# Kernel tuning notes

Hardware: AMD Instinct MI355X
Metric: run time of the kernel (lower is better)

The kernel has to match this reference:

```python
import jax, jax.numpy as jnp
import numpy as np

EPS_D = 1e-05
EPS_LOG = 1e-05
H_BAND = 0.5


def setup_inputs() -> dict:
    key = jax.random.key(0)
    k1, k2 = jax.random.split(key)
    N, C, Hh, Ww = 4, 256, 64, 64
    y = jax.random.normal(k1, (N, C, Hh, Ww), dtype=jnp.float32)
    y_hat = jax.random.normal(k2, (N, C, Hh, Ww), dtype=jnp.float32)
    return {"y": y, "y_hat": y_hat}


def contextual_loss(x, y, h=H_BAND):
    # x, y: (N, C, H, W)
    N, C, Hh, Ww = x.shape
    # mean over W, H, N of y -> per-channel mu, broadcast as (1, C, 1, 1)
    y_mu = y.mean(axis=3).mean(axis=2).mean(axis=0).reshape(1, C, 1, 1)
    x_c = x - y_mu
    y_c = y - y_mu
    x_n = x_c / jnp.linalg.norm(x_c, ord=2, axis=1, keepdims=True)
    y_n = y_c / jnp.linalg.norm(y_c, ord=2, axis=1, keepdims=True)
    x_n = x_n.reshape(N, C, Hh * Ww)  # (N, C, P)
    y_n = y_n.reshape(N, C, Hh * Ww)
    # cosine similarity: (N, P, P)
    cosine_sim = jnp.einsum('ncp,ncq->npq', x_n, y_n)
    d = 1.0 - cosine_sim
    d_min = jnp.min(d, axis=2, keepdims=True)
    d_tilde = d / (d_min + EPS_D)
    w = jnp.exp((1.0 - d_tilde) / h)
    cx_ij = w / jnp.sum(w, axis=2, keepdims=True)
    cx = jnp.mean(jnp.max(cx_ij, axis=1), axis=1)  # (N,)
    return jnp.mean(-jnp.log(cx + EPS_LOG))


def reference(y, y_hat):
    return contextual_loss(y, y_hat)
```

## Files before the change

kernel.cpp:

```cpp
#include <hip/hip_runtime.h>
#include <hip/hip_bf16.h>
#include <math.h>


namespace {
constexpr int NB = 4;
constexpr int C  = 256;
constexpr int P  = 4096;
constexpr float EPSD = 1e-5f;
constexpr float EPSL = 1e-5f;
constexpr float HB   = 0.5f;

constexpr size_t OFF_MU    = 0;
constexpr size_t OFF_XNT   = 256;
constexpr size_t OFF_YNT   = OFF_XNT + (size_t)NB * P * C / 2;
constexpr size_t OFF_XS    = OFF_YNT + (size_t)NB * P * C / 2;
constexpr size_t OFF_RMAXH = OFF_XS + (size_t)NB * P * C / 2;
constexpr size_t OFF_SUMH  = OFF_RMAXH + (size_t)NB * 4 * P;
constexpr size_t OFF_CMAXH = OFF_SUMH + (size_t)NB * 4 * P;
constexpr size_t OFF_RMAX  = OFF_CMAXH + (size_t)NB * 4 * P;
constexpr size_t OFF_ALPHA = OFF_RMAX + (size_t)NB * P;
constexpr size_t OFF_LROW  = OFF_ALPHA + (size_t)NB * P;
}

typedef __attribute__((ext_vector_type(8))) __bf16 bf16x8;
typedef __attribute__((ext_vector_type(16))) float f32x16;
typedef unsigned short u16;

__device__ __forceinline__ bf16x8 ldfrag(const u16* p) {
  return *reinterpret_cast<const bf16x8*>(p);
}
__device__ __forceinline__ void gload_lds16(const u16* g, u16* l) {
  __builtin_amdgcn_global_load_lds(
      (const __attribute__((address_space(1))) void*)g,
      (__attribute__((address_space(3))) void*)l, 16, 0, 0);
}
__device__ __forceinline__ f32x16 zero16() {
  f32x16 z;
#pragma unroll
  for (int i = 0; i < 16; ++i) z[i] = 0.f;
  return z;
}

__device__ __forceinline__ void stage_tile64(const u16* __restrict__ src, int row0,
                                             u16* lds, int t) {
#pragma unroll
  for (int i = 0; i < 8; ++i) {
    const int g  = i * 256 + t;
    const int r  = g >> 5;
    const int gs = (g & 31) ^ (r & 15);
    gload_lds16(src + (size_t)(row0 + r) * 256 + gs * 8, lds + (size_t)g * 8);
  }
}

__global__ void k_mu(const float* __restrict__ yh, float* __restrict__ ws) {
  const int c = blockIdx.x;
  const int t = threadIdx.x;
  float s = 0.f;
  for (int n = 0; n < NB; ++n) {
    const float* base = yh + ((size_t)(n * C + c)) * P;
    for (int p = t; p < P; p += 256) s += base[p];
  }
  __shared__ float red[256];
  red[t] = s;
  __syncthreads();
  for (int w = 128; w > 0; w >>= 1) {
    if (t < w) red[t] += red[t + w];
    __syncthreads();
  }
  if (t == 0) ws[OFF_MU + c] = red[0] * (1.0f / (NB * P));
}

__global__ __launch_bounds__(256) void k_norm(const float* __restrict__ x,
                                              const float* __restrict__ yh,
                                              float* __restrict__ ws) {
  const int b     = blockIdx.x;
  const int arr   = b & 1;
  const int strip = (b >> 1) & 63;
  const int n     = b >> 7;
  const int t     = threadIdx.x;
  const int w     = t >> 6;
  const int l     = t & 63;

  __shared__ float mu_s[C];
  __shared__ float tile[64][257];
  __shared__ float red[4][64];
  __shared__ float invs[64];

  mu_s[t] = ws[OFF_MU + t];
  __syncthreads();

  const float* src = arr ? yh : x;
  const size_t base = ((size_t)n * C) * P + (size_t)strip * 64 + l;
  float ssq = 0.f;
  for (int cc = 0; cc < C; cc += 4) {
    const int c = cc + w;
    const float v = src[base + (size_t)c * P] - mu_s[c];
    tile[l][c] = v;
    ssq += v * v;
  }
  red[w][l] = ssq;
  __syncthreads();
  if (t < 64) invs[t] = 1.0f / sqrtf(red[0][t] + red[1][t] + red[2][t] + red[3][t]);
  __syncthreads();

  uint* dst = reinterpret_cast<uint*>(ws + (arr ? OFF_YNT : OFF_XNT));
  const int c2 = t & 127;
  const size_t drow = ((size_t)n * P + (size_t)strip * 64) * (C / 2);
  for (int it = 0; it < 32; ++it) {
    const int pl = it * 2 + (t >> 7);
    const float s  = invs[pl];
    const float v0 = tile[pl][2 * c2] * s;
    const float v1 = tile[pl][2 * c2 + 1] * s;
    const unsigned short u0 = __builtin_bit_cast(unsigned short, __float2bfloat16(v0));
    const unsigned short u1 = __builtin_bit_cast(unsigned short, __float2bfloat16(v1));
    dst[drow + (size_t)pl * (C / 2) + c2] = ((uint)u1 << 16) | u0;
  }
}

template <int PASS>
__global__ __launch_bounds__(256, 1) void k_rows(float* __restrict__ ws) {
  const int t = threadIdx.x;
  const int wave = t >> 6, l = t & 63, l31 = l & 31, lh = l >> 5, l15 = l31 & 15;
  const int rt = wave >> 1, ct = wave & 1;
  const int bid = blockIdx.x;
  const int qp = bid & 3, n = (bid >> 2) & 3, strip = bid >> 4;
  const int p0 = strip * 128;
  const int qbase = qp * 1024;

  const u16* A = reinterpret_cast<const u16*>(ws + (PASS == 0 ? OFF_XNT : OFF_XS)) +
                 (size_t)n * P * C;
  const u16* yn = reinterpret_cast<const u16*>(ws + OFF_YNT) + (size_t)n * P * C;

  __shared__ __align__(16) u16 Bl[2][64 * 256];

  const u16* Ap0 = A + (size_t)(p0 + rt * 64 + l31) * 256;
  bf16x8 af0[16], af1[16];
#pragma unroll
  for (int ks = 0; ks < 16; ++ks) {
    af0[ks] = ldfrag(Ap0 + (ks * 2 + lh) * 8);
    af1[ks] = ldfrag(Ap0 + 32 * 256 + (ks * 2 + lh) * 8);
  }
  asm volatile("s_waitcnt vmcnt(0)" ::: "memory");
  __builtin_amdgcn_sched_barrier(0);

  float run0[16], run1[16];
#pragma unroll
  for (int r = 0; r < 16; ++r) {
    run0[r] = (PASS == 0) ? -3.0e38f : 0.f;
    run1[r] = (PASS == 0) ? -3.0e38f : 0.f;
  }

  stage_tile64(yn, qbase, Bl[0], t);

  for (int step = 0; step < 16; ++step) {
    if (step + 1 < 16) {
      stage_tile64(yn, qbase + (step + 1) * 64, Bl[(step + 1) & 1], t);
      asm volatile("s_waitcnt vmcnt(8)" ::: "memory");
    } else {
      asm volatile("s_waitcnt vmcnt(0)" ::: "memory");
    }
    __builtin_amdgcn_sched_barrier(0);
    __builtin_amdgcn_s_barrier();
    __builtin_amdgcn_sched_barrier(0);

    const u16* Brow = &Bl[step & 1][(size_t)(ct * 32 + l31) * 256];
    f32x16 a0 = zero16(), a1 = zero16();
    __builtin_amdgcn_s_setprio(1);
#pragma unroll
    for (int ks = 0; ks < 16; ++ks) {
      const bf16x8 bq = ldfrag(Brow + ((ks * 2 + lh) ^ l15) * 8);
      a0 = __builtin_amdgcn_mfma_f32_32x32x16_bf16(af0[ks], bq, a0, 0, 0, 0);
      a1 = __builtin_amdgcn_mfma_f32_32x32x16_bf16(af1[ks], bq, a1, 0, 0, 0);
    }
    __builtin_amdgcn_s_setprio(0);

    if (PASS == 0) {
#pragma unroll
      for (int r = 0; r < 16; ++r) {
        run0[r] = fmaxf(run0[r], a0[r]);
        run1[r] = fmaxf(run1[r], a1[r]);
      }
    } else {
#pragma unroll
      for (int r = 0; r < 16; ++r) {
        run0[r] += __expf(a0[r]);
        run1[r] += __expf(a1[r]);
      }
    }
    __builtin_amdgcn_sched_barrier(0);
    __builtin_amdgcn_s_barrier();
  }

#pragma unroll
  for (int m = 1; m <= 16; m <<= 1) {
#pragma unroll
    for (int r = 0; r < 16; ++r) {
      const float o0 = __shfl_xor(run0[r], m, 64);
      const float o1 = __shfl_xor(run1[r], m, 64);
      run0[r] = (PASS == 0) ? fmaxf(run0[r], o0) : (run0[r] + o0);
      run1[r] = (PASS == 0) ? fmaxf(run1[r], o1) : (run1[r] + o1);
    }
  }
  float (*red)[64] = reinterpret_cast<float(*)[64]>(&Bl[0][0]);
  if (l31 == 0) {
#pragma unroll
    for (int r = 0; r < 16; ++r) {
      const int row = (r & 3) + 8 * (r >> 2) + 4 * lh;
      red[wave][row]      = run0[r];
      red[wave][row + 32] = run1[r];
    }
  }
  __syncthreads();
  if (t < 128) {
    const int rt2 = t >> 6, row = t & 63;
    const float v0 = red[rt2 * 2][row], v1 = red[rt2 * 2 + 1][row];
    const size_t o = (size_t)(n * 4 + qp) * P + p0 + rt2 * 64 + row;
    if (PASS == 0)
      ws[OFF_RMAXH + o] = fmaxf(v0, v1);
    else
      ws[OFF_SUMH + o] = v0 + v1;
  }
}

__global__ void k_alpha(float* __restrict__ ws) {
  const int i = blockIdx.x * 256 + threadIdx.x;
  const int n = i >> 12, p = i & (P - 1);
  float rm = ws[OFF_RMAXH + (size_t)(n * 4) * P + p];
#pragma unroll
  for (int j = 1; j < 4; ++j)
    rm = fmaxf(rm, ws[OFF_RMAXH + (size_t)(n * 4 + j) * P + p]);
  ws[OFF_RMAX + (size_t)n * P + p]  = rm;
  ws[OFF_ALPHA + (size_t)n * P + p] = 1.0f / (HB * (1.0f - rm + EPSD));
}

__global__ __launch_bounds__(256) void k_scale(float* __restrict__ ws) {
  const int g = blockIdx.x * 256 + threadIdx.x;
  const int rowg = g >> 5;
  const int n = rowg >> 12, p = rowg & (P - 1);
  const float a = ws[OFF_ALPHA + (size_t)n * P + p];
  const uint4 v = reinterpret_cast<const uint4*>(ws + OFF_XNT)[g];
  uint4 o;
  uint* vi = (uint*)&v;
  uint* oi = (uint*)&o;
#pragma unroll
  for (int j = 0; j < 4; ++j) {
    const uint u = vi[j];
    const float f0 = __builtin_bit_cast(float, (u & 0xffffu) << 16) * a;
    const float f1 = __builtin_bit_cast(float, (u & 0xffff0000u)) * a;
    const unsigned short b0 = __builtin_bit_cast(unsigned short, __float2bfloat16(f0));
    const unsigned short b1 = __builtin_bit_cast(unsigned short, __float2bfloat16(f1));
    oi[j] = ((uint)b1 << 16) | b0;
  }
  reinterpret_cast<uint4*>(ws + OFF_XS)[g] = o;
}

__global__ void k_L(float* __restrict__ ws) {
  const int i = blockIdx.x * 256 + threadIdx.x;
  const int n = i >> 12, p = i & (P - 1);
  float s = 0.f;
#pragma unroll
  for (int j = 0; j < 4; ++j)
    s += ws[OFF_SUMH + (size_t)(n * 4 + j) * P + p];
  ws[OFF_LROW + (size_t)n * P + p] = logf(s);
}

__global__ __launch_bounds__(256, 1) void k_colp(float* __restrict__ ws) {
  const int t = threadIdx.x;
  const int wave = t >> 6, l = t & 63, l31 = l & 31, lh = l >> 5, l15 = l31 & 15;
  const int rt = wave >> 1, ct = wave & 1;
  const int bid = blockIdx.x;
  const int pp = bid & 3, n = (bid >> 2) & 3, qstrip = bid >> 4;
  const int q0 = qstrip * 128;
  const int pbase = pp * 1024;

  const u16* yn = reinterpret_cast<const u16*>(ws + OFF_YNT) + (size_t)n * P * C;
  const u16* xs = reinterpret_cast<const u16*>(ws + OFF_XS) + (size_t)n * P * C;
  const float* lrw = ws + OFF_LROW + (size_t)n * P;

  __shared__ __align__(16) u16 Bl[2][64 * 256];

  const u16* Ap0 = yn + (size_t)(q0 + rt * 64 + l31) * 256;
  bf16x8 af0[16], af1[16];
#pragma unroll
  for (int ks = 0; ks < 16; ++ks) {
    af0[ks] = ldfrag(Ap0 + (ks * 2 + lh) * 8);
    af1[ks] = ldfrag(Ap0 + 32 * 256 + (ks * 2 + lh) * 8);
  }
  float Lr[16];
#pragma unroll
  for (int s = 0; s < 16; ++s) Lr[s] = lrw[pbase + s * 64 + ct * 32 + l31];

  asm volatile("s_waitcnt vmcnt(0)" ::: "memory");
  __builtin_amdgcn_sched_barrier(0);

  float run0[16], run1[16];
#pragma unroll
  for (int r = 0; r < 16; ++r) { run0[r] = -3.0e38f; run1[r] = -3.0e38f; }

  stage_tile64(xs, pbase, Bl[0], t);

#pragma unroll
  for (int step = 0; step < 16; ++step) {
    if (step + 1 < 16) {
      stage_tile64(xs, pbase + (step + 1) * 64, Bl[(step + 1) & 1], t);
      asm volatile("s_waitcnt vmcnt(8)" ::: "memory");
    } else {
      asm volatile("s_waitcnt vmcnt(0)" ::: "memory");
    }
    __builtin_amdgcn_sched_barrier(0);
    __builtin_amdgcn_s_barrier();
    __builtin_amdgcn_sched_barrier(0);

    const float L_ = Lr[step];

    const u16* Brow = &Bl[step & 1][(size_t)(ct * 32 + l31) * 256];
    f32x16 a0 = zero16(), a1 = zero16();
    __builtin_amdgcn_s_setprio(1);
#pragma unroll
    for (int ks = 0; ks < 16; ++ks) {
      const bf16x8 bq = ldfrag(Brow + ((ks * 2 + lh) ^ l15) * 8);
      a0 = __builtin_amdgcn_mfma_f32_32x32x16_bf16(af0[ks], bq, a0, 0, 0, 0);
      a1 = __builtin_amdgcn_mfma_f32_32x32x16_bf16(af1[ks], bq, a1, 0, 0, 0);
    }
    __builtin_amdgcn_s_setprio(0);
#pragma unroll
    for (int r = 0; r < 16; ++r) {
      run0[r] = fmaxf(run0[r], a0[r] - L_);
      run1[r] = fmaxf(run1[r], a1[r] - L_);
    }
    __builtin_amdgcn_sched_barrier(0);
    __builtin_amdgcn_s_barrier();
  }

#pragma unroll
  for (int m = 1; m <= 16; m <<= 1) {
#pragma unroll
    for (int r = 0; r < 16; ++r) {
      run0[r] = fmaxf(run0[r], __shfl_xor(run0[r], m, 64));
      run1[r] = fmaxf(run1[r], __shfl_xor(run1[r], m, 64));
    }
  }
  float (*red)[64] = reinterpret_cast<float(*)[64]>(&Bl[0][0]);
  if (l31 == 0) {
#pragma unroll
    for (int r = 0; r < 16; ++r) {
      const int row = (r & 3) + 8 * (r >> 2) + 4 * lh;
      red[wave][row]      = run0[r];
      red[wave][row + 32] = run1[r];
    }
  }
  __syncthreads();
  if (t < 128) {
    const int rt2 = t >> 6, row = t & 63;
    const float v = fmaxf(red[rt2 * 2][row], red[rt2 * 2 + 1][row]);
    ws[OFF_CMAXH + (size_t)(n * 4 + pp) * P + q0 + rt2 * 64 + row] = v;
  }
}

__global__ void k_final(const float* __restrict__ ws, float* __restrict__ out) {
  const int t = threadIdx.x;
  __shared__ float red[256];
  __shared__ float lsum_s;
  if (t == 0) lsum_s = 0.f;
  for (int n = 0; n < NB; ++n) {
    float e = 0.f;
    for (int q = t; q < P; q += 256) {
      float m = ws[OFF_CMAXH + (size_t)(n * 4) * P + q];
#pragma unroll
      for (int j = 1; j < 4; ++j)
        m = fmaxf(m, ws[OFF_CMAXH + (size_t)(n * 4 + j) * P + q]);
      e += __expf(m);
    }
    __syncthreads();
    red[t] = e;
    __syncthreads();
    for (int w = 128; w > 0; w >>= 1) {
      if (t < w) red[t] += red[t + w];
      __syncthreads();
    }
    if (t == 0) lsum_s += -logf(red[0] * (1.0f / P) + EPSL);
  }
  __syncthreads();
  if (t == 0) out[0] = lsum_s * 0.25f;
}

extern "C" void kernel_launch(void* const* d_in, const int* in_sizes, int n_in,
                              void* d_out, int out_size, void* d_ws, size_t ws_size,
                              hipStream_t stream) {
  const float* x  = (const float*)d_in[0];
  const float* yh = (const float*)d_in[1];
  float* ws  = (float*)d_ws;
  float* out = (float*)d_out;

  k_mu<<<dim3(C), dim3(256), 0, stream>>>(yh, ws);
  k_norm<<<dim3(NB * 64 * 2), dim3(256), 0, stream>>>(x, yh, ws);
  k_rows<0><<<dim3(512), dim3(256), 0, stream>>>(ws);
  k_alpha<<<dim3(NB * P / 256), dim3(256), 0, stream>>>(ws);
  k_scale<<<dim3(NB * P * C / 8 / 256), dim3(256), 0, stream>>>(ws);
  k_rows<1><<<dim3(512), dim3(256), 0, stream>>>(ws);
  k_L<<<dim3(NB * P / 256), dim3(256), 0, stream>>>(ws);
  k_colp<<<dim3(512), dim3(256), 0, stream>>>(ws);
  k_final<<<dim3(1), dim3(256), 0, stream>>>(ws, out);
}
```

Measured before the change: 206.8 us.

## Shrink GEMM tiles to 128x32 per step and split columns eight ways

The three MFMA-based passes (row max, row exp-sum, column max) now give each wave a single 32-row A fragment against a 32-column B tile instead of two fragments against a 64-column tile. The column range is split into eight parts instead of four, doubling the grid to 1024 blocks, and partial results go straight to global memory without an LDS cross-wave reduction. The setprio hints are dropped and the per-step log terms move from registers into LDS. This cuts register and LDS use per block, which may allow higher occupancy and more parallelism. In exchange each B tile is reused by half as many MFMAs, global staging traffic roughly doubles, and the downstream reductions must combine eight partials instead of four.

```diff
diff --git a/kernel.cpp b/kernel.cpp
--- a/kernel.cpp
+++ b/kernel.cpp
@@ -16,9 +16,9 @@
 constexpr size_t OFF_YNT   = OFF_XNT + (size_t)NB * P * C / 2;
 constexpr size_t OFF_XS    = OFF_YNT + (size_t)NB * P * C / 2;
 constexpr size_t OFF_RMAXH = OFF_XS + (size_t)NB * P * C / 2;
-constexpr size_t OFF_SUMH  = OFF_RMAXH + (size_t)NB * 4 * P;
-constexpr size_t OFF_CMAXH = OFF_SUMH + (size_t)NB * 4 * P;
-constexpr size_t OFF_RMAX  = OFF_CMAXH + (size_t)NB * 4 * P;
+constexpr size_t OFF_SUMH  = OFF_RMAXH + (size_t)NB * 8 * P;
+constexpr size_t OFF_CMAXH = OFF_SUMH + (size_t)NB * 8 * P;
+constexpr size_t OFF_RMAX  = OFF_CMAXH + (size_t)NB * 8 * P;
 constexpr size_t OFF_ALPHA = OFF_RMAX + (size_t)NB * P;
 constexpr size_t OFF_LROW  = OFF_ALPHA + (size_t)NB * P;
 }
@@ -42,10 +42,10 @@
   return z;
 }
 
-__device__ __forceinline__ void stage_tile64(const u16* __restrict__ src, int row0,
+__device__ __forceinline__ void stage_tile32(const u16* __restrict__ src, int row0,
                                              u16* lds, int t) {
 #pragma unroll
-  for (int i = 0; i < 8; ++i) {
+  for (int i = 0; i < 4; ++i) {
     const int g  = i * 256 + t;
     const int r  = g >> 5;
     const int gs = (g & 31) ^ (r & 15);
@@ -122,41 +122,34 @@
 __global__ __launch_bounds__(256, 1) void k_rows(float* __restrict__ ws) {
   const int t = threadIdx.x;
   const int wave = t >> 6, l = t & 63, l31 = l & 31, lh = l >> 5, l15 = l31 & 15;
-  const int rt = wave >> 1, ct = wave & 1;
   const int bid = blockIdx.x;
-  const int qp = bid & 3, n = (bid >> 2) & 3, strip = bid >> 4;
+  const int part = bid & 7, n = (bid >> 3) & 3, strip = bid >> 5;
   const int p0 = strip * 128;
-  const int qbase = qp * 1024;
+  const int qbase = part * 512;
 
   const u16* A = reinterpret_cast<const u16*>(ws + (PASS == 0 ? OFF_XNT : OFF_XS)) +
                  (size_t)n * P * C;
   const u16* yn = reinterpret_cast<const u16*>(ws + OFF_YNT) + (size_t)n * P * C;
 
-  __shared__ __align__(16) u16 Bl[2][64 * 256];
-
-  const u16* Ap0 = A + (size_t)(p0 + rt * 64 + l31) * 256;
-  bf16x8 af0[16], af1[16];
-#pragma unroll
-  for (int ks = 0; ks < 16; ++ks) {
-    af0[ks] = ldfrag(Ap0 + (ks * 2 + lh) * 8);
-    af1[ks] = ldfrag(Ap0 + 32 * 256 + (ks * 2 + lh) * 8);
-  }
+  __shared__ __align__(16) u16 Bl[2][32 * 256];
+
+  const u16* Ap = A + (size_t)(p0 + wave * 32 + l31) * 256;
+  bf16x8 af[16];
+#pragma unroll
+  for (int ks = 0; ks < 16; ++ks) af[ks] = ldfrag(Ap + (ks * 2 + lh) * 8);
   asm volatile("s_waitcnt vmcnt(0)" ::: "memory");
   __builtin_amdgcn_sched_barrier(0);
 
-  float run0[16], run1[16];
-#pragma unroll
-  for (int r = 0; r < 16; ++r) {
-    run0[r] = (PASS == 0) ? -3.0e38f : 0.f;
-    run1[r] = (PASS == 0) ? -3.0e38f : 0.f;
-  }
-
-  stage_tile64(yn, qbase, Bl[0], t);
+  float run[16];
+#pragma unroll
+  for (int r = 0; r < 16; ++r) run[r] = (PASS == 0) ? -3.0e38f : 0.f;
+
+  stage_tile32(yn, qbase, Bl[0], t);
 
   for (int step = 0; step < 16; ++step) {
     if (step + 1 < 16) {
-      stage_tile64(yn, qbase + (step + 1) * 64, Bl[(step + 1) & 1], t);
-      asm volatile("s_waitcnt vmcnt(8)" ::: "memory");
+      stage_tile32(yn, qbase + (step + 1) * 32, Bl[(step + 1) & 1], t);
+      asm volatile("s_waitcnt vmcnt(4)" ::: "memory");
     } else {
       asm volatile("s_waitcnt vmcnt(0)" ::: "memory");
     }
@@ -164,29 +157,20 @@
     __builtin_amdgcn_s_barrier();
     __builtin_amdgcn_sched_barrier(0);
 
-    const u16* Brow = &Bl[step & 1][(size_t)(ct * 32 + l31) * 256];
-    f32x16 a0 = zero16(), a1 = zero16();
-    __builtin_amdgcn_s_setprio(1);
+    const u16* Brow = &Bl[step & 1][(size_t)l31 * 256];
+    f32x16 acc = zero16();
 #pragma unroll
     for (int ks = 0; ks < 16; ++ks) {
       const bf16x8 bq = ldfrag(Brow + ((ks * 2 + lh) ^ l15) * 8);
-      a0 = __builtin_amdgcn_mfma_f32_32x32x16_bf16(af0[ks], bq, a0, 0, 0, 0);
-      a1 = __builtin_amdgcn_mfma_f32_32x32x16_bf16(af1[ks], bq, a1, 0, 0, 0);
-    }
-    __builtin_amdgcn_s_setprio(0);
+      acc = __builtin_amdgcn_mfma_f32_32x32x16_bf16(af[ks], bq, acc, 0, 0, 0);
+    }
 
     if (PASS == 0) {
 #pragma unroll
-      for (int r = 0; r < 16; ++r) {
-        run0[r] = fmaxf(run0[r], a0[r]);
-        run1[r] = fmaxf(run1[r], a1[r]);
-      }
+      for (int r = 0; r < 16; ++r) run[r] = fmaxf(run[r], acc[r]);
     } else {
 #pragma unroll
-      for (int r = 0; r < 16; ++r) {
-        run0[r] += __expf(a0[r]);
-        run1[r] += __expf(a1[r]);
-      }
+      for (int r = 0; r < 16; ++r) run[r] += __expf(acc[r]);
     }
     __builtin_amdgcn_sched_barrier(0);
     __builtin_amdgcn_s_barrier();
@@ -196,40 +180,30 @@
   for (int m = 1; m <= 16; m <<= 1) {
 #pragma unroll
     for (int r = 0; r < 16; ++r) {
-      const float o0 = __shfl_xor(run0[r], m, 64);
-      const float o1 = __shfl_xor(run1[r], m, 64);
-      run0[r] = (PASS == 0) ? fmaxf(run0[r], o0) : (run0[r] + o0);
-      run1[r] = (PASS == 0) ? fmaxf(run1[r], o1) : (run1[r] + o1);
-    }
-  }
-  float (*red)[64] = reinterpret_cast<float(*)[64]>(&Bl[0][0]);
+      const float o = __shfl_xor(run[r], m, 64);
+      run[r] = (PASS == 0) ? fmaxf(run[r], o) : (run[r] + o);
+    }
+  }
   if (l31 == 0) {
+    const size_t ob = (size_t)(n * 8 + part) * P + p0 + wave * 32;
 #pragma unroll
     for (int r = 0; r < 16; ++r) {
       const int row = (r & 3) + 8 * (r >> 2) + 4 * lh;
-      red[wave][row]      = run0[r];
-      red[wave][row + 32] = run1[r];
-    }
-  }
-  __syncthreads();
-  if (t < 128) {
-    const int rt2 = t >> 6, row = t & 63;
-    const float v0 = red[rt2 * 2][row], v1 = red[rt2 * 2 + 1][row];
-    const size_t o = (size_t)(n * 4 + qp) * P + p0 + rt2 * 64 + row;
-    if (PASS == 0)
-      ws[OFF_RMAXH + o] = fmaxf(v0, v1);
-    else
-      ws[OFF_SUMH + o] = v0 + v1;
+      if (PASS == 0)
+        ws[OFF_RMAXH + ob + row] = run[r];
+      else
+        ws[OFF_SUMH + ob + row] = run[r];
+    }
   }
 }
 
 __global__ void k_alpha(float* __restrict__ ws) {
   const int i = blockIdx.x * 256 + threadIdx.x;
   const int n = i >> 12, p = i & (P - 1);
-  float rm = ws[OFF_RMAXH + (size_t)(n * 4) * P + p];
-#pragma unroll
-  for (int j = 1; j < 4; ++j)
-    rm = fmaxf(rm, ws[OFF_RMAXH + (size_t)(n * 4 + j) * P + p]);
+  float rm = ws[OFF_RMAXH + (size_t)(n * 8) * P + p];
+#pragma unroll
+  for (int j = 1; j < 8; ++j)
+    rm = fmaxf(rm, ws[OFF_RMAXH + (size_t)(n * 8 + j) * P + p]);
   ws[OFF_RMAX + (size_t)n * P + p]  = rm;
   ws[OFF_ALPHA + (size_t)n * P + p] = 1.0f / (HB * (1.0f - rm + EPSD));
 }
@@ -260,51 +234,44 @@
   const int n = i >> 12, p = i & (P - 1);
   float s = 0.f;
 #pragma unroll
-  for (int j = 0; j < 4; ++j)
-    s += ws[OFF_SUMH + (size_t)(n * 4 + j) * P + p];
+  for (int j = 0; j < 8; ++j)
+    s += ws[OFF_SUMH + (size_t)(n * 8 + j) * P + p];
   ws[OFF_LROW + (size_t)n * P + p] = logf(s);
 }
 
 __global__ __launch_bounds__(256, 1) void k_colp(float* __restrict__ ws) {
   const int t = threadIdx.x;
   const int wave = t >> 6, l = t & 63, l31 = l & 31, lh = l >> 5, l15 = l31 & 15;
-  const int rt = wave >> 1, ct = wave & 1;
   const int bid = blockIdx.x;
-  const int pp = bid & 3, n = (bid >> 2) & 3, qstrip = bid >> 4;
+  const int part = bid & 7, n = (bid >> 3) & 3, qstrip = bid >> 5;
   const int q0 = qstrip * 128;
-  const int pbase = pp * 1024;
+  const int pbase = part * 512;
 
   const u16* yn = reinterpret_cast<const u16*>(ws + OFF_YNT) + (size_t)n * P * C;
   const u16* xs = reinterpret_cast<const u16*>(ws + OFF_XS) + (size_t)n * P * C;
   const float* lrw = ws + OFF_LROW + (size_t)n * P;
 
-  __shared__ __align__(16) u16 Bl[2][64 * 256];
-
-  const u16* Ap0 = yn + (size_t)(q0 + rt * 64 + l31) * 256;
-  bf16x8 af0[16], af1[16];
-#pragma unroll
-  for (int ks = 0; ks < 16; ++ks) {
-    af0[ks] = ldfrag(Ap0 + (ks * 2 + lh) * 8);
-    af1[ks] = ldfrag(Ap0 + 32 * 256 + (ks * 2 + lh) * 8);
-  }
-  float Lr[16];
-#pragma unroll
-  for (int s = 0; s < 16; ++s) Lr[s] = lrw[pbase + s * 64 + ct * 32 + l31];
-
-  asm volatile("s_waitcnt vmcnt(0)" ::: "memory");
-  __builtin_amdgcn_sched_barrier(0);
-
-  float run0[16], run1[16];
-#pragma unroll
-  for (int r = 0; r < 16; ++r) { run0[r] = -3.0e38f; run1[r] = -3.0e38f; }
-
-  stage_tile64(xs, pbase, Bl[0], t);
-
-#pragma unroll
+  __shared__ __align__(16) u16 Bl[2][32 * 256];
+  __shared__ float Lsh[512];
+
+  const u16* Ap = yn + (size_t)(q0 + wave * 32 + l31) * 256;
+  bf16x8 af[16];
+#pragma unroll
+  for (int ks = 0; ks < 16; ++ks) af[ks] = ldfrag(Ap + (ks * 2 + lh) * 8);
+
+  for (int i = t; i < 512; i += 256) Lsh[i] = lrw[pbase + i];
+  __syncthreads();
+
+  float run[16];
+#pragma unroll
+  for (int r = 0; r < 16; ++r) run[r] = -3.0e38f;
+
+  stage_tile32(xs, pbase, Bl[0], t);
+
   for (int step = 0; step < 16; ++step) {
     if (step + 1 < 16) {
-      stage_tile64(xs, pbase + (step + 1) * 64, Bl[(step + 1) & 1], t);
-      asm volatile("s_waitcnt vmcnt(8)" ::: "memory");
+      stage_tile32(xs, pbase + (step + 1) * 32, Bl[(step + 1) & 1], t);
+      asm volatile("s_waitcnt vmcnt(4)" ::: "memory");
     } else {
       asm volatile("s_waitcnt vmcnt(0)" ::: "memory");
     }
@@ -312,23 +279,18 @@
     __builtin_amdgcn_s_barrier();
     __builtin_amdgcn_sched_barrier(0);
 
-    const float L_ = Lr[step];
-
-    const u16* Brow = &Bl[step & 1][(size_t)(ct * 32 + l31) * 256];
-    f32x16 a0 = zero16(), a1 = zero16();
-    __builtin_amdgcn_s_setprio(1);
+    const float L_ = Lsh[step * 32 + l31];
+
+    const u16* Brow = &Bl[step & 1][(size_t)l31 * 256];
+    f32x16 acc = zero16();
 #pragma unroll
     for (int ks = 0; ks < 16; ++ks) {
       const bf16x8 bq = ldfrag(Brow + ((ks * 2 + lh) ^ l15) * 8);
-      a0 = __builtin_amdgcn_mfma_f32_32x32x16_bf16(af0[ks], bq, a0, 0, 0, 0);
-      a1 = __builtin_amdgcn_mfma_f32_32x32x16_bf16(af1[ks], bq, a1, 0, 0, 0);
-    }
-    __builtin_amdgcn_s_setprio(0);
-#pragma unroll
-    for (int r = 0; r < 16; ++r) {
-      run0[r] = fmaxf(run0[r], a0[r] - L_);
-      run1[r] = fmaxf(run1[r], a1[r] - L_);
-    }
+      acc = __builtin_amdgcn_mfma_f32_32x32x16_bf16(af[ks], bq, acc, 0, 0, 0);
+    }
+#pragma unroll
+    for (int r = 0; r < 16; ++r) run[r] = fmaxf(run[r], acc[r] - L_);
+
     __builtin_amdgcn_sched_barrier(0);
     __builtin_amdgcn_s_barrier();
   }
@@ -336,25 +298,15 @@
 #pragma unroll
   for (int m = 1; m <= 16; m <<= 1) {
 #pragma unroll
-    for (int r = 0; r < 16; ++r) {
-      run0[r] = fmaxf(run0[r], __shfl_xor(run0[r], m, 64));
-      run1[r] = fmaxf(run1[r], __shfl_xor(run1[r], m, 64));
-    }
-  }
-  float (*red)[64] = reinterpret_cast<float(*)[64]>(&Bl[0][0]);
+    for (int r = 0; r < 16; ++r) run[r] = fmaxf(run[r], __shfl_xor(run[r], m, 64));
+  }
   if (l31 == 0) {
+    const size_t ob = (size_t)(n * 8 + part) * P + q0 + wave * 32;
 #pragma unroll
     for (int r = 0; r < 16; ++r) {
       const int row = (r & 3) + 8 * (r >> 2) + 4 * lh;
-      red[wave][row]      = run0[r];
-      red[wave][row + 32] = run1[r];
-    }
-  }
-  __syncthreads();
-  if (t < 128) {
-    const int rt2 = t >> 6, row = t & 63;
-    const float v = fmaxf(red[rt2 * 2][row], red[rt2 * 2 + 1][row]);
-    ws[OFF_CMAXH + (size_t)(n * 4 + pp) * P + q0 + rt2 * 64 + row] = v;
+      ws[OFF_CMAXH + ob + row] = run[r];
+    }
   }
 }
 
@@ -366,10 +318,10 @@
   for (int n = 0; n < NB; ++n) {
     float e = 0.f;
     for (int q = t; q < P; q += 256) {
-      float m = ws[OFF_CMAXH + (size_t)(n * 4) * P + q];
-#pragma unroll
-      for (int j = 1; j < 4; ++j)
-        m = fmaxf(m, ws[OFF_CMAXH + (size_t)(n * 4 + j) * P + q]);
+      float m = ws[OFF_CMAXH + (size_t)(n * 8) * P + q];
+#pragma unroll
+      for (int j = 1; j < 8; ++j)
+        m = fmaxf(m, ws[OFF_CMAXH + (size_t)(n * 8 + j) * P + q]);
       e += __expf(m);
     }
     __syncthreads();
@@ -395,11 +347,11 @@
 
   k_mu<<<dim3(C), dim3(256), 0, stream>>>(yh, ws);
   k_norm<<<dim3(NB * 64 * 2), dim3(256), 0, stream>>>(x, yh, ws);
-  k_rows<0><<<dim3(512), dim3(256), 0, stream>>>(ws);
+  k_rows<0><<<dim3(1024), dim3(256), 0, stream>>>(ws);
   k_alpha<<<dim3(NB * P / 256), dim3(256), 0, stream>>>(ws);
   k_scale<<<dim3(NB * P * C / 8 / 256), dim3(256), 0, stream>>>(ws);
-  k_rows<1><<<dim3(512), dim3(256), 0, stream>>>(ws);
+  k_rows<1><<<dim3(1024), dim3(256), 0, stream>>>(ws);
   k_L<<<dim3(NB * P / 256), dim3(256), 0, stream>>>(ws);
-  k_colp<<<dim3(512), dim3(256), 0, stream>>>(ws);
+  k_colp<<<dim3(1024), dim3(256), 0, stream>>>(ws);
   k_final<<<dim3(1), dim3(256), 0, stream>>>(ws, out);
 }
```

After: 210.2 us. About the same (+1.7%).
